# Optimization experiments

Hardware: AMD Instinct MI355X
Metric: run time of the kernel (lower is better)

The kernel has to match this reference:

```python
import jax, jax.numpy as jnp
import numpy as np

NUM_HEADS = 12
HEAD_SIZE = 64
N_EMBED = 768
SEQ_LEN = 2048
BATCH = 4


def setup_inputs() -> dict:
    key = jax.random.key(0)
    ks = jax.random.split(key, 7)
    s = 0.02
    x = jax.random.normal(ks[0], (BATCH, SEQ_LEN, N_EMBED), dtype=jnp.float32)
    # per-head bias-free q/k/v projections: [H, E, D]
    Wq = jax.random.normal(ks[1], (NUM_HEADS, N_EMBED, HEAD_SIZE), dtype=jnp.float32) * s
    Wk = jax.random.normal(ks[2], (NUM_HEADS, N_EMBED, HEAD_SIZE), dtype=jnp.float32) * s
    Wv = jax.random.normal(ks[3], (NUM_HEADS, N_EMBED, HEAD_SIZE), dtype=jnp.float32) * s
    # output projection: Linear(num_heads*head_size, n_embed)
    Wp = jax.random.normal(ks[4], (NUM_HEADS * HEAD_SIZE, N_EMBED), dtype=jnp.float32) * s
    bp = jax.random.normal(ks[5], (N_EMBED,), dtype=jnp.float32) * s
    return {"x": x, "Wq": Wq, "Wk": Wk, "Wv": Wv, "Wp": Wp, "bp": bp}


def reference(x, Wq, Wk, Wv, Wp, bp):
    B, S, E = x.shape
    scale = HEAD_SIZE ** -0.5
    # project all heads at once: [B,H,S,D]
    q = jnp.einsum("bse,hed->bhsd", x, Wq)
    k = jnp.einsum("bse,hed->bhsd", x, Wk)
    v = jnp.einsum("bse,hed->bhsd", x, Wv)
    # scaled dot-product scores [B,H,S,S] with causal mask
    scores = jnp.einsum("bhsd,bhtd->bhst", q, k) * scale
    causal = jnp.tril(jnp.ones((S, S), dtype=bool))
    scores = jnp.where(causal[None, None, :, :], scores, jnp.finfo(scores.dtype).min)
    attn = jax.nn.softmax(scores, axis=-1)
    out = jnp.einsum("bhst,bhtd->bhsd", attn, v)
    # concat heads along feature dim: [B,S,H*D]
    out = out.transpose(0, 2, 1, 3).reshape(B, S, NUM_HEADS * HEAD_SIZE)
    # final projection (dropout rate = 0.0)
    return out @ Wp + bp
```

## Files before the change

### kernel.cpp

```cpp
#include <hip/hip_runtime.h>
#include <hip/hip_bf16.h>


typedef __attribute__((ext_vector_type(8))) short bf16x8;
typedef __attribute__((ext_vector_type(4))) float f32x4;
typedef __attribute__((ext_vector_type(16))) float f32x16;
typedef __attribute__((ext_vector_type(4))) uint u32x4;

#define OFF_XB   0
#define OFF_WT   6291456
#define OFF_WPT  8060928
#define OFF_QKV  8650752
#define OFF_AO   27525120

#define SCALE_LOG2E 0.1803368801111204f

__device__ inline ushort f2bf(float f) {
  __hip_bfloat16 h = __float2bfloat16(f);
  return *reinterpret_cast<ushort*>(&h);
}
__device__ inline uint cvt_pk(float lo, float hi) {
  uint r;
  asm("v_cvt_pk_bf16_f32 %0, %1, %2" : "=v"(r) : "v"(lo), "v"(hi));
  return r;
}
#define GLOAD16(g, l)                                                              \
  __builtin_amdgcn_global_load_lds(                                                \
      (const __attribute__((address_space(1))) uint*)(g),                          \
      (__attribute__((address_space(3))) uint*)(l), 16, 0, 0)

#define WAITBAR(n) asm volatile("s_waitcnt vmcnt(" #n ")\ns_barrier" ::: "memory")
#define ENDBAR()   asm volatile("s_waitcnt lgkmcnt(0)\ns_barrier" ::: "memory")

__global__ __launch_bounds__(256) void cvt_bf16(const float* __restrict__ src,
                                                ushort* __restrict__ dst, int n8) {
  int i = blockIdx.x * 256 + threadIdx.x;
  if (i >= n8) return;
  float4 a = *(const float4*)&src[(size_t)i * 8];
  float4 b = *(const float4*)&src[(size_t)i * 8 + 4];
  u32x4 pk = {cvt_pk(a.x, a.y), cvt_pk(a.z, a.w), cvt_pk(b.x, b.y), cvt_pk(b.z, b.w)};
  *(bf16x8*)&dst[(size_t)i * 8] = __builtin_bit_cast(bf16x8, pk);
}

__global__ __launch_bounds__(256) void transpose_w(const float* __restrict__ src,
                                                   ushort* __restrict__ dst,
                                                   int Edim, int Ddim) {
  __shared__ ushort tile[64][130];
  int mat = blockIdx.y;
  int ntd = Ddim >> 6;
  int te = blockIdx.x / ntd, td = blockIdx.x % ntd;
  size_t base = (size_t)mat * Edim * Ddim;
  int t = threadIdx.x;
#pragma unroll
  for (int i = 0; i < 16; i++) {
    int idx = i * 256 + t;
    int r = idx >> 6, c = idx & 63;
    tile[r][c] = f2bf(src[base + (size_t)(te * 64 + r) * Ddim + td * 64 + c]);
  }
  __syncthreads();
#pragma unroll
  for (int i = 0; i < 16; i++) {
    int idx = i * 256 + t;
    int c = idx >> 6, r = idx & 63;
    dst[base + (size_t)(td * 64 + c) * Edim + te * 64 + r] = tile[r][c];
  }
}

__device__ inline uint swz(uint row) { return (row + (row >> 2)) & 3; }

__global__ __launch_bounds__(256) void gemm_qkv(const ushort* __restrict__ X,
                                                const ushort* __restrict__ Wt,
                                                ushort* __restrict__ qkv,
                                                uint* __restrict__ vtg) {
  __shared__ ushort Ash[2][128 * 32];
  __shared__ ushort Bsh[2][128 * 32];
  int mb = blockIdx.x, nb = blockIdx.y;
  int t = threadIdx.x, w = t >> 6, lane = t & 63, lo = lane & 15, g = lane >> 4;
  int wr = w >> 1, wc = w & 1;
  const ushort* Ab = X + (size_t)mb * 128 * 768;
  const ushort* Bb = Wt + (size_t)nb * 128 * 768;
  f32x4 acc[4][4];
#pragma unroll
  for (int fi = 0; fi < 4; fi++)
#pragma unroll
    for (int fj = 0; fj < 4; fj++) acc[fi][fj] = (f32x4){0.f, 0.f, 0.f, 0.f};
  uint ci0 = w * 128 + lane, ci1 = w * 128 + 64 + lane;
  uint row0 = ci0 >> 2, sc0 = ((ci0 & 3) ^ swz(ci0 >> 2)) << 4;
  uint row1 = ci1 >> 2, sc1 = ((ci1 & 3) ^ swz(ci1 >> 2)) << 4;

#define QKV_STAGE(tile, bsel)                                                        \
  {                                                                                  \
    int e0 = (tile) * 32;                                                            \
    GLOAD16((const char*)(Ab + (size_t)row0 * 768 + e0) + sc0, &Ash[bsel][(w * 128) * 8]);      \
    GLOAD16((const char*)(Bb + (size_t)row0 * 768 + e0) + sc0, &Bsh[bsel][(w * 128) * 8]);      \
    GLOAD16((const char*)(Ab + (size_t)row1 * 768 + e0) + sc1, &Ash[bsel][(w * 128 + 64) * 8]); \
    GLOAD16((const char*)(Bb + (size_t)row1 * 768 + e0) + sc1, &Bsh[bsel][(w * 128 + 64) * 8]); \
  }

  QKV_STAGE(0, 0);
  QKV_STAGE(1, 1);
  uint rsw = swz(lo) << 4;
  for (int it = 0; it < 24; ++it) {
    if (it < 23) { WAITBAR(4); } else { WAITBAR(0); }
    const ushort* Acur = Ash[it & 1];
    const ushort* Bcur = Bsh[it & 1];
    bf16x8 af[4], bf[4];
#pragma unroll
    for (int fi = 0; fi < 4; fi++) {
      int arow = wr * 64 + fi * 16 + lo;
      af[fi] = *(const bf16x8*)((const char*)Acur + arow * 64 + ((g << 4) ^ rsw));
      int brow = wc * 64 + fi * 16 + lo;
      bf[fi] = *(const bf16x8*)((const char*)Bcur + brow * 64 + ((g << 4) ^ rsw));
    }
#pragma unroll
    for (int fi = 0; fi < 4; fi++)
#pragma unroll
      for (int fj = 0; fj < 4; fj++)
        acc[fi][fj] = __builtin_amdgcn_mfma_f32_16x16x32_bf16(af[fi], bf[fj], acc[fi][fj], 0, 0, 0);
    if (it < 22) {
      ENDBAR();
      QKV_STAGE(it + 2, it & 1);
    }
  }
#undef QKV_STAGE
  int mat = nb * 2 + wc;
  int ty = mat / 12, h = mat % 12;
  if (ty < 2) {
#pragma unroll
    for (int fi = 0; fi < 4; fi++)
#pragma unroll
      for (int fj = 0; fj < 4; fj++) {
        int d = fj * 16 + lo;
#pragma unroll
        for (int rr = 0; rr < 4; rr++) {
          int m = mb * 128 + wr * 64 + fi * 16 + g * 4 + rr;
          int b = m >> 11, s = m & 2047;
          qkv[(size_t)ty * 6291456 + (size_t)(b * 12 + h) * 131072 + (size_t)s * 64 + d] =
              f2bf(acc[fi][fj][rr]);
        }
      }
  } else {
#pragma unroll
    for (int fi = 0; fi < 4; fi++)
#pragma unroll
      for (int fj = 0; fj < 4; fj++) {
        int d = fj * 16 + lo;
#pragma unroll
        for (int rr = 0; rr < 4; rr += 2) {
          int m = mb * 128 + wr * 64 + fi * 16 + g * 4 + rr;
          int b = m >> 11, s = m & 2047;
          uint pk = cvt_pk(acc[fi][fj][rr], acc[fi][fj][rr + 1]);
          vtg[(size_t)(b * 12 + h) * 65536 + (s >> 6) * 2048 + d * 32 + ((s & 63) >> 1)] = pk;
        }
      }
  }
}

__global__ __launch_bounds__(256, 3) void attn_fwd(const ushort* __restrict__ Qg,
                                                   const ushort* __restrict__ Kg,
                                                   const uint* __restrict__ Vtg,
                                                   ushort* __restrict__ ao) {
  __shared__ ushort Ksh[2][64 * 72];
  __shared__ uint Vsh[2][64 * 36];
  int x = blockIdx.x;
  int head = x % 48;
  int qb = 15 - x / 48;
  int T = 2 * qb + 2;
  int t = threadIdx.x, w = t >> 6, q31 = t & 31, hi = (t & 63) >> 5;
  const ushort* Q = Qg + (size_t)head * 131072;
  const ushort* K = Kg + (size_t)head * 131072;
  const uint* V = Vtg + (size_t)head * 65536;
  int qstart = qb * 128 + 32 * w;
  int qg = qstart + q31;
  bf16x8 qf[4];
#pragma unroll
  for (int s = 0; s < 4; s++)
    qf[s] = *(const bf16x8*)&Q[(size_t)qg * 64 + s * 16 + hi * 8];
  bf16x8 ones;
#pragma unroll
  for (int i = 0; i < 8; i++) ones[i] = (short)0x3F80;
  f32x16 oacc[2], lacc;
#pragma unroll
  for (int r = 0; r < 16; r++) { oacc[0][r] = 0.f; oacc[1][r] = 0.f; lacc[r] = 0.f; }
  int sr = t >> 3, sc = t & 7;
  bf16x8 kreg[2];
  u32x4 vreg[2];
#pragma unroll
  for (int i = 0; i < 2; i++) {
    kreg[i] = *(const bf16x8*)&K[(size_t)(i * 32 + sr) * 64 + sc * 8];
    vreg[i] = *(const u32x4*)&V[(i * 32 + sr) * 32 + sc * 4];
  }
#pragma unroll
  for (int i = 0; i < 2; i++) {
    *(bf16x8*)&Ksh[0][(i * 32 + sr) * 72 + sc * 8] = kreg[i];
    *(u32x4*)&Vsh[0][(i * 32 + sr) * 36 + sc * 4] = vreg[i];
  }
  for (int kb = 0; kb < T; kb++) {
    __syncthreads();
    if (kb + 1 < T) {
      int t1 = (kb + 1) * 64;
#pragma unroll
      for (int i = 0; i < 2; i++) {
        kreg[i] = *(const bf16x8*)&K[(size_t)(t1 + i * 32 + sr) * 64 + sc * 8];
        vreg[i] = *(const u32x4*)&V[(kb + 1) * 2048 + (i * 32 + sr) * 32 + sc * 4];
      }
    }
    int t0 = kb * 64;
    if (t0 <= qstart + 31) {
      const ushort* Kb = Ksh[kb & 1];
      const uint* Vb = Vsh[kb & 1];
      bool act1 = (t0 + 32 <= qstart + 31);
      f32x16 st0, st1;
#pragma unroll
      for (int r = 0; r < 16; r++) { st0[r] = 0.f; st1[r] = 0.f; }
#pragma unroll
      for (int s = 0; s < 4; s++) {
        bf16x8 kf = *(const bf16x8*)&Kb[q31 * 72 + s * 16 + hi * 8];
        st0 = __builtin_amdgcn_mfma_f32_32x32x16_bf16(kf, qf[s], st0, 0, 0, 0);
      }
      if (act1) {
#pragma unroll
        for (int s = 0; s < 4; s++) {
          bf16x8 kf = *(const bf16x8*)&Kb[(32 + q31) * 72 + s * 16 + hi * 8];
          st1 = __builtin_amdgcn_mfma_f32_32x32x16_bf16(kf, qf[s], st1, 0, 0, 0);
        }
      }
      if (t0 + 31 > qstart) {
        int base = t0 - qstart;
#pragma unroll
        for (int r = 0; r < 16; r++) {
          int crow = (r & 3) + 8 * (r >> 2) + 4 * hi;
          if (base + crow > q31) st0[r] = -3e38f;
        }
      }
      if (act1 && (t0 + 63 > qstart)) {
        int base = t0 + 32 - qstart;
#pragma unroll
        for (int r = 0; r < 16; r++) {
          int crow = (r & 3) + 8 * (r >> 2) + 4 * hi;
          if (base + crow > q31) st1[r] = -3e38f;
        }
      }
#pragma unroll
      for (int r = 0; r < 16; r++)
        st0[r] = __builtin_amdgcn_exp2f(st0[r] * SCALE_LOG2E);
      if (act1) {
#pragma unroll
        for (int r = 0; r < 16; r++)
          st1[r] = __builtin_amdgcn_exp2f(st1[r] * SCALE_LOG2E);
      }
      int ns = act1 ? 4 : 2;
      bf16x8 paf[4];
#pragma unroll
      for (int s = 0; s < 4; s++) {
        if (s < ns) {
          const f32x16& sv = (s < 2) ? st0 : st1;
          int rb = (s & 1) * 8;
          uint a = cvt_pk(sv[rb + 0], sv[rb + 1]);
          uint b2 = cvt_pk(sv[rb + 2], sv[rb + 3]);
          uint c = cvt_pk(sv[rb + 4], sv[rb + 5]);
          uint d = cvt_pk(sv[rb + 6], sv[rb + 7]);
          asm volatile("v_permlane32_swap_b32 %0, %1" : "+v"(a), "+v"(c));
          asm volatile("v_permlane32_swap_b32 %0, %1" : "+v"(b2), "+v"(d));
          u32x4 u4 = {a, b2, c, d};
          paf[s] = __builtin_bit_cast(bf16x8, u4);
        }
      }
#pragma unroll
      for (int s = 0; s < 4; s++) {
        if (s < ns) {
          lacc = __builtin_amdgcn_mfma_f32_32x32x16_bf16(paf[s], ones, lacc, 0, 0, 0);
#pragma unroll
          for (int dt = 0; dt < 2; dt++) {
            bf16x8 vf = *(const bf16x8*)&Vb[(dt * 32 + q31) * 36 + s * 8 + hi * 4];
            oacc[dt] = __builtin_amdgcn_mfma_f32_32x32x16_bf16(paf[s], vf, oacc[dt], 0, 0, 0);
          }
        }
      }
    }
    if (kb + 1 < T) {
      int b2 = (kb + 1) & 1;
#pragma unroll
      for (int i = 0; i < 2; i++) {
        *(bf16x8*)&Ksh[b2][(i * 32 + sr) * 72 + sc * 8] = kreg[i];
        *(u32x4*)&Vsh[b2][(i * 32 + sr) * 36 + sc * 4] = vreg[i];
      }
    }
  }
  int hh = head % 12, bb = head / 12;
#pragma unroll
  for (int dt = 0; dt < 2; dt++)
#pragma unroll
    for (int r = 0; r < 16; r++) {
      int qr = qstart + (r & 3) + 8 * (r >> 2) + 4 * hi;
      ao[(size_t)(bb * 2048 + qr) * 768 + hh * 64 + dt * 32 + q31] =
          f2bf(oacc[dt][r] / lacc[r]);
    }
}

__global__ __launch_bounds__(128) void gemm_out(const ushort* __restrict__ A,
                                                const ushort* __restrict__ Bt,
                                                const float* __restrict__ bias,
                                                float* __restrict__ out) {
  __shared__ ushort Ash[2][128 * 32];
  __shared__ ushort Bsh[2][64 * 32];
  int mb = blockIdx.x, nb = blockIdx.y;
  int t = threadIdx.x, w = t >> 6, lane = t & 63, lo = lane & 15, g = lane >> 4;
  const ushort* Ab = A + (size_t)mb * 128 * 768;
  const ushort* Bb = Bt + (size_t)nb * 64 * 768;
  f32x4 acc[4][4];
#pragma unroll
  for (int fi = 0; fi < 4; fi++)
#pragma unroll
    for (int fj = 0; fj < 4; fj++) acc[fi][fj] = (f32x4){0.f, 0.f, 0.f, 0.f};
  uint aci[4], asc[4], bci[2], bsc[2];
#pragma unroll
  for (int j = 0; j < 4; j++) {
    uint ci = w * 256 + j * 64 + lane;
    aci[j] = ci;
    asc[j] = ((ci & 3) ^ swz(ci >> 2)) << 4;
  }
#pragma unroll
  for (int j = 0; j < 2; j++) {
    uint ci = w * 128 + j * 64 + lane;
    bci[j] = ci;
    bsc[j] = ((ci & 3) ^ swz(ci >> 2)) << 4;
  }

#define OUT_STAGE(tile, bsel)                                                          \
  {                                                                                    \
    int e0 = (tile) * 32;                                                              \
    _Pragma("unroll")                                                                  \
    for (int j = 0; j < 4; j++)                                                        \
      GLOAD16((const char*)(Ab + (size_t)(aci[j] >> 2) * 768 + e0) + asc[j],           \
              &Ash[bsel][(w * 256 + j * 64) * 8]);                                     \
    _Pragma("unroll")                                                                  \
    for (int j = 0; j < 2; j++)                                                        \
      GLOAD16((const char*)(Bb + (size_t)(bci[j] >> 2) * 768 + e0) + bsc[j],           \
              &Bsh[bsel][(w * 128 + j * 64) * 8]);                                     \
  }

  OUT_STAGE(0, 0);
  OUT_STAGE(1, 1);
  uint rsw = swz(lo) << 4;
  for (int it = 0; it < 24; ++it) {
    if (it < 23) { WAITBAR(6); } else { WAITBAR(0); }
    const ushort* Acur = Ash[it & 1];
    const ushort* Bcur = Bsh[it & 1];
    bf16x8 af[4], bf[4];
#pragma unroll
    for (int fi = 0; fi < 4; fi++) {
      int arow = w * 64 + fi * 16 + lo;
      af[fi] = *(const bf16x8*)((const char*)Acur + arow * 64 + ((g << 4) ^ rsw));
      int brow = fi * 16 + lo;
      bf[fi] = *(const bf16x8*)((const char*)Bcur + brow * 64 + ((g << 4) ^ rsw));
    }
#pragma unroll
    for (int fi = 0; fi < 4; fi++)
#pragma unroll
      for (int fj = 0; fj < 4; fj++)
        acc[fi][fj] = __builtin_amdgcn_mfma_f32_16x16x32_bf16(af[fi], bf[fj], acc[fi][fj], 0, 0, 0);
    if (it < 22) {
      ENDBAR();
      OUT_STAGE(it + 2, it & 1);
    }
  }
#undef OUT_STAGE
#pragma unroll
  for (int fj = 0; fj < 4; fj++) {
    int col = nb * 64 + fj * 16 + lo;
    float bv = bias[col];
#pragma unroll
    for (int fi = 0; fi < 4; fi++)
#pragma unroll
      for (int rr = 0; rr < 4; rr++) {
        int m = mb * 128 + w * 64 + fi * 16 + g * 4 + rr;
        out[(size_t)m * 768 + col] = acc[fi][fj][rr] + bv;
      }
  }
}

extern "C" void kernel_launch(void* const* d_in, const int* in_sizes, int n_in,
                              void* d_out, int out_size, void* d_ws, size_t ws_size,
                              hipStream_t stream) {
  const float* x  = (const float*)d_in[0];
  const float* Wq = (const float*)d_in[1];
  const float* Wk = (const float*)d_in[2];
  const float* Wv = (const float*)d_in[3];
  const float* Wp = (const float*)d_in[4];
  const float* bp = (const float*)d_in[5];
  float* out = (float*)d_out;
  ushort* ws = (ushort*)d_ws;

  ushort* xb  = ws + OFF_XB;
  ushort* wt  = ws + OFF_WT;
  ushort* wpt = ws + OFF_WPT;
  ushort* qkv = ws + OFF_QKV;
  uint*   vt  = (uint*)(ws + OFF_QKV + 2 * 6291456);
  ushort* ao  = ws + OFF_AO;

  cvt_bf16<<<dim3(3072), 256, 0, stream>>>(x, xb, 786432);
  transpose_w<<<dim3(12, 12), 256, 0, stream>>>(Wq, wt + 0 * 589824, 768, 64);
  transpose_w<<<dim3(12, 12), 256, 0, stream>>>(Wk, wt + 1 * 589824, 768, 64);
  transpose_w<<<dim3(12, 12), 256, 0, stream>>>(Wv, wt + 2 * 589824, 768, 64);
  transpose_w<<<dim3(144, 1), 256, 0, stream>>>(Wp, wpt, 768, 768);

  gemm_qkv<<<dim3(64, 18), 256, 0, stream>>>(xb, wt, qkv, vt);
  attn_fwd<<<dim3(768), 256, 0, stream>>>(qkv, qkv + 6291456, vt, ao);
  gemm_out<<<dim3(64, 12), 128, 0, stream>>>(ao, wpt, bp, out);
}
```

Before: 133.7 us.

## Use 2-wave 128x128 tiles in QKV/out GEMMs and merge weight transposes

The QKV GEMM moves from 4 waves on a 128x128 tile to 2 waves, each computing a 64x128 sub-tile. This doubles per-wave B-fragment reuse and MFMA work per LDS read. The output GEMM widens its N tile from 64 to 128, which halves the grid and raises A-tile reuse. The three Q/K/V weight-transpose launches are merged into one kernel to cut launch overhead. Both GEMMs now hold 128 accumulator floats per thread and the grids are smaller, so register pressure and lower occupancy or parallelism are the risks.

After: 129.4 us. -3.2%, faster.

```diff
diff --git a/kernel.cpp b/kernel.cpp
--- a/kernel.cpp
+++ b/kernel.cpp
@@ -42,80 +42,114 @@
   *(bf16x8*)&dst[(size_t)i * 8] = __builtin_bit_cast(bf16x8, pk);
 }
 
+__global__ __launch_bounds__(256) void transpose_wqkv(const float* __restrict__ Wq,
+                                                      const float* __restrict__ Wk,
+                                                      const float* __restrict__ Wv,
+                                                      ushort* __restrict__ dst) {
+  __shared__ ushort tile[64][130];
+  int mat = blockIdx.y;
+  int te = blockIdx.x;
+  const float* src = (mat < 12) ? Wq : (mat < 24) ? Wk : Wv;
+  int m12 = mat % 12;
+  size_t base = (size_t)m12 * 768 * 64;
+  int t = threadIdx.x;
+#pragma unroll
+  for (int i = 0; i < 16; i++) {
+    int idx = i * 256 + t;
+    int r = idx >> 6, c = idx & 63;
+    tile[r][c] = f2bf(src[base + (size_t)(te * 64 + r) * 64 + c]);
+  }
+  __syncthreads();
+  size_t obase = (size_t)mat * 49152;
+#pragma unroll
+  for (int i = 0; i < 16; i++) {
+    int idx = i * 256 + t;
+    int c = idx >> 6, r = idx & 63;
+    dst[obase + (size_t)c * 768 + te * 64 + r] = tile[r][c];
+  }
+}
+
 __global__ __launch_bounds__(256) void transpose_w(const float* __restrict__ src,
                                                    ushort* __restrict__ dst,
                                                    int Edim, int Ddim) {
   __shared__ ushort tile[64][130];
-  int mat = blockIdx.y;
   int ntd = Ddim >> 6;
   int te = blockIdx.x / ntd, td = blockIdx.x % ntd;
-  size_t base = (size_t)mat * Edim * Ddim;
   int t = threadIdx.x;
 #pragma unroll
   for (int i = 0; i < 16; i++) {
     int idx = i * 256 + t;
     int r = idx >> 6, c = idx & 63;
-    tile[r][c] = f2bf(src[base + (size_t)(te * 64 + r) * Ddim + td * 64 + c]);
+    tile[r][c] = f2bf(src[(size_t)(te * 64 + r) * Ddim + td * 64 + c]);
   }
   __syncthreads();
 #pragma unroll
   for (int i = 0; i < 16; i++) {
     int idx = i * 256 + t;
     int c = idx >> 6, r = idx & 63;
-    dst[base + (size_t)(td * 64 + c) * Edim + te * 64 + r] = tile[r][c];
+    dst[(size_t)(td * 64 + c) * Edim + te * 64 + r] = tile[r][c];
   }
 }
 
 __device__ inline uint swz(uint row) { return (row + (row >> 2)) & 3; }
 
-__global__ __launch_bounds__(256) void gemm_qkv(const ushort* __restrict__ X,
-                                                const ushort* __restrict__ Wt,
-                                                ushort* __restrict__ qkv,
-                                                uint* __restrict__ vtg) {
+__global__ __launch_bounds__(128, 2) void gemm_qkv(const ushort* __restrict__ X,
+                                                   const ushort* __restrict__ Wt,
+                                                   ushort* __restrict__ qkv,
+                                                   uint* __restrict__ vtg) {
   __shared__ ushort Ash[2][128 * 32];
   __shared__ ushort Bsh[2][128 * 32];
   int mb = blockIdx.x, nb = blockIdx.y;
   int t = threadIdx.x, w = t >> 6, lane = t & 63, lo = lane & 15, g = lane >> 4;
-  int wr = w >> 1, wc = w & 1;
   const ushort* Ab = X + (size_t)mb * 128 * 768;
   const ushort* Bb = Wt + (size_t)nb * 128 * 768;
-  f32x4 acc[4][4];
+  f32x4 acc[4][8];
 #pragma unroll
   for (int fi = 0; fi < 4; fi++)
 #pragma unroll
-    for (int fj = 0; fj < 4; fj++) acc[fi][fj] = (f32x4){0.f, 0.f, 0.f, 0.f};
-  uint ci0 = w * 128 + lane, ci1 = w * 128 + 64 + lane;
-  uint row0 = ci0 >> 2, sc0 = ((ci0 & 3) ^ swz(ci0 >> 2)) << 4;
-  uint row1 = ci1 >> 2, sc1 = ((ci1 & 3) ^ swz(ci1 >> 2)) << 4;
-
-#define QKV_STAGE(tile, bsel)                                                        \
-  {                                                                                  \
-    int e0 = (tile) * 32;                                                            \
-    GLOAD16((const char*)(Ab + (size_t)row0 * 768 + e0) + sc0, &Ash[bsel][(w * 128) * 8]);      \
-    GLOAD16((const char*)(Bb + (size_t)row0 * 768 + e0) + sc0, &Bsh[bsel][(w * 128) * 8]);      \
-    GLOAD16((const char*)(Ab + (size_t)row1 * 768 + e0) + sc1, &Ash[bsel][(w * 128 + 64) * 8]); \
-    GLOAD16((const char*)(Bb + (size_t)row1 * 768 + e0) + sc1, &Bsh[bsel][(w * 128 + 64) * 8]); \
+    for (int fj = 0; fj < 8; fj++) acc[fi][fj] = (f32x4){0.f, 0.f, 0.f, 0.f};
+  uint srow[4], ssc[4];
+#pragma unroll
+  for (int j = 0; j < 4; j++) {
+    uint ci = j * 128 + t;
+    srow[j] = ci >> 2;
+    ssc[j] = ((ci & 3) ^ swz(ci >> 2)) << 4;
+  }
+
+#define QKV_STAGE(tile, bsel)                                                         \
+  {                                                                                   \
+    int e0 = (tile) * 32;                                                             \
+    _Pragma("unroll")                                                                 \
+    for (int j = 0; j < 4; j++) {                                                     \
+      GLOAD16((const char*)(Ab + (size_t)srow[j] * 768 + e0) + ssc[j],                \
+              &Ash[bsel][(j * 128 + w * 64) * 8]);                                    \
+      GLOAD16((const char*)(Bb + (size_t)srow[j] * 768 + e0) + ssc[j],                \
+              &Bsh[bsel][(j * 128 + w * 64) * 8]);                                    \
+    }                                                                                 \
   }
 
   QKV_STAGE(0, 0);
   QKV_STAGE(1, 1);
   uint rsw = swz(lo) << 4;
   for (int it = 0; it < 24; ++it) {
-    if (it < 23) { WAITBAR(4); } else { WAITBAR(0); }
+    if (it < 23) { WAITBAR(8); } else { WAITBAR(0); }
     const ushort* Acur = Ash[it & 1];
     const ushort* Bcur = Bsh[it & 1];
-    bf16x8 af[4], bf[4];
+    bf16x8 af[4], bf[8];
 #pragma unroll
     for (int fi = 0; fi < 4; fi++) {
-      int arow = wr * 64 + fi * 16 + lo;
+      int arow = w * 64 + fi * 16 + lo;
       af[fi] = *(const bf16x8*)((const char*)Acur + arow * 64 + ((g << 4) ^ rsw));
-      int brow = wc * 64 + fi * 16 + lo;
-      bf[fi] = *(const bf16x8*)((const char*)Bcur + brow * 64 + ((g << 4) ^ rsw));
+    }
+#pragma unroll
+    for (int fj = 0; fj < 8; fj++) {
+      int brow = fj * 16 + lo;
+      bf[fj] = *(const bf16x8*)((const char*)Bcur + brow * 64 + ((g << 4) ^ rsw));
     }
 #pragma unroll
     for (int fi = 0; fi < 4; fi++)
 #pragma unroll
-      for (int fj = 0; fj < 4; fj++)
+      for (int fj = 0; fj < 8; fj++)
         acc[fi][fj] = __builtin_amdgcn_mfma_f32_16x16x32_bf16(af[fi], bf[fj], acc[fi][fj], 0, 0, 0);
     if (it < 22) {
       ENDBAR();
@@ -123,36 +157,32 @@
     }
   }
 #undef QKV_STAGE
-  int mat = nb * 2 + wc;
-  int ty = mat / 12, h = mat % 12;
-  if (ty < 2) {
-#pragma unroll
-    for (int fi = 0; fi < 4; fi++)
-#pragma unroll
-      for (int fj = 0; fj < 4; fj++) {
-        int d = fj * 16 + lo;
+#pragma unroll
+  for (int fj = 0; fj < 8; fj++) {
+    int mat = nb * 2 + (fj >> 2);
+    int ty = mat / 12, h = mat % 12;
+    int d = (fj & 3) * 16 + lo;
+    if (ty < 2) {
+#pragma unroll
+      for (int fi = 0; fi < 4; fi++)
 #pragma unroll
         for (int rr = 0; rr < 4; rr++) {
-          int m = mb * 128 + wr * 64 + fi * 16 + g * 4 + rr;
+          int m = mb * 128 + w * 64 + fi * 16 + g * 4 + rr;
           int b = m >> 11, s = m & 2047;
           qkv[(size_t)ty * 6291456 + (size_t)(b * 12 + h) * 131072 + (size_t)s * 64 + d] =
               f2bf(acc[fi][fj][rr]);
         }
-      }
-  } else {
-#pragma unroll
-    for (int fi = 0; fi < 4; fi++)
-#pragma unroll
-      for (int fj = 0; fj < 4; fj++) {
-        int d = fj * 16 + lo;
+    } else {
+#pragma unroll
+      for (int fi = 0; fi < 4; fi++)
 #pragma unroll
         for (int rr = 0; rr < 4; rr += 2) {
-          int m = mb * 128 + wr * 64 + fi * 16 + g * 4 + rr;
+          int m = mb * 128 + w * 64 + fi * 16 + g * 4 + rr;
           int b = m >> 11, s = m & 2047;
           uint pk = cvt_pk(acc[fi][fj][rr], acc[fi][fj][rr + 1]);
           vtg[(size_t)(b * 12 + h) * 65536 + (s >> 6) * 2048 + d * 32 + ((s & 63) >> 1)] = pk;
         }
-      }
+    }
   }
 }
 
@@ -298,67 +328,63 @@
     }
 }
 
-__global__ __launch_bounds__(128) void gemm_out(const ushort* __restrict__ A,
-                                                const ushort* __restrict__ Bt,
-                                                const float* __restrict__ bias,
-                                                float* __restrict__ out) {
+__global__ __launch_bounds__(128, 2) void gemm_out(const ushort* __restrict__ A,
+                                                   const ushort* __restrict__ Bt,
+                                                   const float* __restrict__ bias,
+                                                   float* __restrict__ out) {
   __shared__ ushort Ash[2][128 * 32];
-  __shared__ ushort Bsh[2][64 * 32];
+  __shared__ ushort Bsh[2][128 * 32];
   int mb = blockIdx.x, nb = blockIdx.y;
   int t = threadIdx.x, w = t >> 6, lane = t & 63, lo = lane & 15, g = lane >> 4;
   const ushort* Ab = A + (size_t)mb * 128 * 768;
-  const ushort* Bb = Bt + (size_t)nb * 64 * 768;
-  f32x4 acc[4][4];
+  const ushort* Bb = Bt + (size_t)nb * 128 * 768;
+  f32x4 acc[4][8];
 #pragma unroll
   for (int fi = 0; fi < 4; fi++)
 #pragma unroll
-    for (int fj = 0; fj < 4; fj++) acc[fi][fj] = (f32x4){0.f, 0.f, 0.f, 0.f};
-  uint aci[4], asc[4], bci[2], bsc[2];
+    for (int fj = 0; fj < 8; fj++) acc[fi][fj] = (f32x4){0.f, 0.f, 0.f, 0.f};
+  uint srow[4], ssc[4];
 #pragma unroll
   for (int j = 0; j < 4; j++) {
-    uint ci = w * 256 + j * 64 + lane;
-    aci[j] = ci;
-    asc[j] = ((ci & 3) ^ swz(ci >> 2)) << 4;
-  }
-#pragma unroll
-  for (int j = 0; j < 2; j++) {
-    uint ci = w * 128 + j * 64 + lane;
-    bci[j] = ci;
-    bsc[j] = ((ci & 3) ^ swz(ci >> 2)) << 4;
-  }
-
-#define OUT_STAGE(tile, bsel)                                                          \
-  {                                                                                    \
-    int e0 = (tile) * 32;                                                              \
-    _Pragma("unroll")                                                                  \
-    for (int j = 0; j < 4; j++)                                                        \
-      GLOAD16((const char*)(Ab + (size_t)(aci[j] >> 2) * 768 + e0) + asc[j],           \
-              &Ash[bsel][(w * 256 + j * 64) * 8]);                                     \
-    _Pragma("unroll")                                                                  \
-    for (int j = 0; j < 2; j++)                                                        \
-      GLOAD16((const char*)(Bb + (size_t)(bci[j] >> 2) * 768 + e0) + bsc[j],           \
-              &Bsh[bsel][(w * 128 + j * 64) * 8]);                                     \
+    uint ci = j * 128 + t;
+    srow[j] = ci >> 2;
+    ssc[j] = ((ci & 3) ^ swz(ci >> 2)) << 4;
+  }
+
+#define OUT_STAGE(tile, bsel)                                                         \
+  {                                                                                   \
+    int e0 = (tile) * 32;                                                             \
+    _Pragma("unroll")                                                                 \
+    for (int j = 0; j < 4; j++) {                                                     \
+      GLOAD16((const char*)(Ab + (size_t)srow[j] * 768 + e0) + ssc[j],                \
+              &Ash[bsel][(j * 128 + w * 64) * 8]);                                    \
+      GLOAD16((const char*)(Bb + (size_t)srow[j] * 768 + e0) + ssc[j],                \
+              &Bsh[bsel][(j * 128 + w * 64) * 8]);                                    \
+    }                                                                                 \
   }
 
   OUT_STAGE(0, 0);
   OUT_STAGE(1, 1);
   uint rsw = swz(lo) << 4;
   for (int it = 0; it < 24; ++it) {
-    if (it < 23) { WAITBAR(6); } else { WAITBAR(0); }
+    if (it < 23) { WAITBAR(8); } else { WAITBAR(0); }
     const ushort* Acur = Ash[it & 1];
     const ushort* Bcur = Bsh[it & 1];
-    bf16x8 af[4], bf[4];
+    bf16x8 af[4], bf[8];
 #pragma unroll
     for (int fi = 0; fi < 4; fi++) {
       int arow = w * 64 + fi * 16 + lo;
       af[fi] = *(const bf16x8*)((const char*)Acur + arow * 64 + ((g << 4) ^ rsw));
-      int brow = fi * 16 + lo;
-      bf[fi] = *(const bf16x8*)((const char*)Bcur + brow * 64 + ((g << 4) ^ rsw));
+    }
+#pragma unroll
+    for (int fj = 0; fj < 8; fj++) {
+      int brow = fj * 16 + lo;
+      bf[fj] = *(const bf16x8*)((const char*)Bcur + brow * 64 + ((g << 4) ^ rsw));
     }
 #pragma unroll
     for (int fi = 0; fi < 4; fi++)
 #pragma unroll
-      for (int fj = 0; fj < 4; fj++)
+      for (int fj = 0; fj < 8; fj++)
         acc[fi][fj] = __builtin_amdgcn_mfma_f32_16x16x32_bf16(af[fi], bf[fj], acc[fi][fj], 0, 0, 0);
     if (it < 22) {
       ENDBAR();
@@ -367,8 +393,8 @@
   }
 #undef OUT_STAGE
 #pragma unroll
-  for (int fj = 0; fj < 4; fj++) {
-    int col = nb * 64 + fj * 16 + lo;
+  for (int fj = 0; fj < 8; fj++) {
+    int col = nb * 128 + fj * 16 + lo;
     float bv = bias[col];
 #pragma unroll
     for (int fi = 0; fi < 4; fi++)
@@ -400,12 +426,10 @@
   ushort* ao  = ws + OFF_AO;
 
   cvt_bf16<<<dim3(3072), 256, 0, stream>>>(x, xb, 786432);
-  transpose_w<<<dim3(12, 12), 256, 0, stream>>>(Wq, wt + 0 * 589824, 768, 64);
-  transpose_w<<<dim3(12, 12), 256, 0, stream>>>(Wk, wt + 1 * 589824, 768, 64);
-  transpose_w<<<dim3(12, 12), 256, 0, stream>>>(Wv, wt + 2 * 589824, 768, 64);
-  transpose_w<<<dim3(144, 1), 256, 0, stream>>>(Wp, wpt, 768, 768);
-
-  gemm_qkv<<<dim3(64, 18), 256, 0, stream>>>(xb, wt, qkv, vt);
+  transpose_wqkv<<<dim3(12, 36), 256, 0, stream>>>(Wq, Wk, Wv, wt);
+  transpose_w<<<dim3(144), 256, 0, stream>>>(Wp, wpt, 768, 768);
+
+  gemm_qkv<<<dim3(64, 18), 128, 0, stream>>>(xb, wt, qkv, vt);
   attn_fwd<<<dim3(768), 256, 0, stream>>>(qkv, qkv + 6291456, vt, ao);
-  gemm_out<<<dim3(64, 12), 128, 0, stream>>>(ao, wpt, bp, out);
-}
+  gemm_out<<<dim3(64, 6), 128, 0, stream>>>(ao, wpt, bp, out);
+}
```
